# Kernel tuning notes

Hardware: AMD Instinct MI355X
Metric: run time of the kernel (lower is better)

Reference implementation:

```python
import jax, jax.numpy as jnp
import numpy as np

B, S, D = 4, 2048, 1024
H = 16
DK = D // H  # 64
F = 4096


def layer_norm(x, g, b, eps=1e-5):
    mu = jnp.mean(x, axis=-1, keepdims=True)
    var = jnp.mean(jnp.square(x - mu), axis=-1, keepdims=True)
    return (x - mu) * jax.lax.rsqrt(var + eps) * g + b


def setup_inputs() -> dict:
    key = jax.random.key(0)
    ks = jax.random.split(key, 12)
    s_in = 1.0 / np.sqrt(D)
    s_ff = 1.0 / np.sqrt(F)
    return {
        "x": jax.random.normal(ks[0], (B, S, D), jnp.float32),
        # per-head Q/K/V projections stacked: [H, D, DK]
        "Wq": jax.random.normal(ks[1], (H, D, DK), jnp.float32) * s_in,
        "bq": jnp.zeros((H, DK), jnp.float32),
        "Wk": jax.random.normal(ks[2], (H, D, DK), jnp.float32) * s_in,
        "bk": jnp.zeros((H, DK), jnp.float32),
        "Wv": jax.random.normal(ks[3], (H, D, DK), jnp.float32) * s_in,
        "bv": jnp.zeros((H, DK), jnp.float32),
        # output projection: [H*DK, D]
        "Wo": jax.random.normal(ks[4], (H * DK, D), jnp.float32) * s_in,
        "bo": jnp.zeros((D,), jnp.float32),
        "ln1_g": jnp.ones((D,), jnp.float32),
        "ln1_b": jnp.zeros((D,), jnp.float32),
        # FFN
        "W1": jax.random.normal(ks[5], (D, F), jnp.float32) * s_in,
        "b1": jnp.zeros((F,), jnp.float32),
        "W2": jax.random.normal(ks[6], (F, D), jnp.float32) * s_ff,
        "b2": jnp.zeros((D,), jnp.float32),
        "ln2_g": jnp.ones((D,), jnp.float32),
        "ln2_b": jnp.zeros((D,), jnp.float32),
    }


def reference(x, Wq, bq, Wk, bk, Wv, bv, Wo, bo, ln1_g, ln1_b,
              W1, b1, W2, b2, ln2_g, ln2_b):
    # --- multi-head attention (self-attention: q = k = v = x) ---
    q = jnp.einsum("bsd,hdk->bhsk", x, Wq) + bq[:, None, :]
    k = jnp.einsum("bsd,hdk->bhsk", x, Wk) + bk[:, None, :]
    v = jnp.einsum("bsd,hdk->bhsk", x, Wv) + bv[:, None, :]
    scale = 1.0 / jnp.sqrt(jnp.asarray(DK, x.dtype))
    scores = jnp.einsum("bhsk,bhtk->bhst", q, k) * scale  # [B,H,S,S]
    attn = jax.nn.softmax(scores, axis=-1)
    ctx = jnp.einsum("bhst,bhtk->bhsk", attn, v)           # [B,H,S,DK]
    # concat heads -> [B,S,H*DK], output projection
    ctx = jnp.transpose(ctx, (0, 2, 1, 3)).reshape(B, S, H * DK)
    attn_out = ctx @ Wo + bo
    # residual + post-LN (dropout is identity in eval mode)
    h = layer_norm(x + attn_out, ln1_g, ln1_b)
    # --- feed-forward (tanh activation) ---
    ff = jnp.tanh(h @ W1 + b1) @ W2 + b2
    return layer_norm(h + ff, ln2_g, ln2_b)
```

## Files before the change

### kernel.cpp

```cpp
#include <hip/hip_runtime.h>
#include <hip/hip_bf16.h>
#include <math.h>

typedef __attribute__((ext_vector_type(8))) short short8;
typedef __attribute__((ext_vector_type(4))) float f32x4;

#define NB 4
#define NS 2048
#define ND 1024
#define NH 16
#define NDK 64
#define NF 4096
#define NM (NB*NS)

#define QSCALE 0.18033688f
#define SMAX 32.0f

__device__ __forceinline__ unsigned short f2b(float f) {
  union { __hip_bfloat16 h; unsigned short u; } c;
  c.h = __float2bfloat16(f);
  return c.u;
}

__device__ __forceinline__ float b2f(unsigned short u) {
  union { float f; unsigned int i; } c;
  c.i = ((unsigned int)u) << 16;
  return c.f;
}

__device__ __forceinline__ void gload_lds16(const void* g, void* l) {
  __builtin_amdgcn_global_load_lds((const __attribute__((address_space(1))) void*)g,
                                   (__attribute__((address_space(3))) void*)l,
                                   16, 0, 0);
}

__device__ __forceinline__ float fast_tanh(float x) {
  float e = __builtin_amdgcn_exp2f(x * 2.885390082f);
  return 1.0f - 2.0f * __builtin_amdgcn_rcpf(e + 1.0f);
}


__global__ __launch_bounds__(256)
void cvt_f32_bf16(const float* __restrict__ in, unsigned short* __restrict__ out, int n4) {
  int i = blockIdx.x * 256 + threadIdx.x;
  if (i >= n4) return;
  float4 v = ((const float4*)in)[i];
  ushort4 o;
  o.x = f2b(v.x); o.y = f2b(v.y); o.z = f2b(v.z); o.w = f2b(v.w);
  ((ushort4*)out)[i] = o;
}

__global__ __launch_bounds__(256)
void transpose_generic(const float* __restrict__ src, unsigned short* __restrict__ dst,
                       int ldsrc, int lddst) {
  __shared__ float t[32][33];
  int k0 = blockIdx.x * 32, n0 = blockIdx.y * 32;
  int tx = threadIdx.x, ty = threadIdx.y;
  for (int r = ty; r < 32; r += 8)
    t[r][tx] = src[(size_t)(k0 + r) * ldsrc + n0 + tx];
  __syncthreads();
  for (int r = ty; r < 32; r += 8)
    dst[(size_t)(n0 + r) * lddst + k0 + tx] = f2b(t[tx][r]);
}

__global__ __launch_bounds__(256)
void transpose_qkv(const float* __restrict__ Wq, const float* __restrict__ Wk,
                   const float* __restrict__ Wv, unsigned short* __restrict__ dst) {
  int z = blockIdx.z, which = z / 16, h = z % 16;
  const float* src = (which == 0 ? Wq : which == 1 ? Wk : Wv) + (size_t)h * ND * NDK;
  float scale = (which == 0) ? QSCALE : 1.0f;
  unsigned short* d = dst + (size_t)(which * 1024 + h * 64) * ND;
  __shared__ float t[32][33];
  int k0 = blockIdx.x * 32, n0 = blockIdx.y * 32;
  int tx = threadIdx.x, ty = threadIdx.y;
  for (int r = ty; r < 32; r += 8)
    t[r][tx] = src[(size_t)(k0 + r) * NDK + n0 + tx];
  __syncthreads();
  for (int r = ty; r < 32; r += 8)
    d[(size_t)(n0 + r) * ND + k0 + tx] = f2b(t[tx][r] * scale);
}

__global__ __launch_bounds__(256)
void pack_bias(const float* __restrict__ bq, const float* __restrict__ bk,
               const float* __restrict__ bv, float* __restrict__ out) {
  int i = blockIdx.x * 256 + threadIdx.x;
  if (i >= 3072) return;
  float v = (i < 1024) ? bq[i] * QSCALE : (i < 2048 ? bk[i - 1024] : bv[i - 2048]);
  out[i] = v;
}

__global__ __launch_bounds__(256)
void transpose_v(const unsigned short* __restrict__ qkv, unsigned short* __restrict__ vt) {
  __shared__ unsigned short t[32][33];
  int bh = blockIdx.z; int b = bh >> 4, h = bh & 15;
  int s0 = blockIdx.x * 32;
  int d0 = blockIdx.y * 32;
  int tx = threadIdx.x, ty = threadIdx.y;
  for (int r = ty; r < 32; r += 8)
    t[r][tx] = qkv[(size_t)(b * NS + s0 + r) * 3072 + 2048 + h * 64 + d0 + tx];
  __syncthreads();
  for (int r = ty; r < 32; r += 8)
    vt[((size_t)bh * 64 + d0 + r) * NS + s0 + tx] = t[tx][r];
}


template<int EPI>
__global__ __launch_bounds__(256)
void gemm_bt(const unsigned short* __restrict__ A, const unsigned short* __restrict__ Bt,
             const float* __restrict__ bias, void* __restrict__ Cout,
             int M, int N, int K)
{
  __shared__ __align__(16) unsigned short As[128 * 64];
  __shared__ __align__(16) unsigned short Bs[128 * 64];

  const int id = blockIdx.x;
  const int xcd = id & 7;
  const int s = id >> 3;
  const int nbPerX = (N >> 7) >> 3;
  const int nb = xcd * nbPerX + (s % nbPerX);
  const int mb = s / nbPerX;
  const int n0 = nb * 128;
  const int m0 = mb * 128;

  const int tid = threadIdx.x;
  const int wave = tid >> 6, lane = tid & 63;
  const int l16 = lane & 15, lhi = lane >> 4;
  const int wr = wave >> 1, wc = wave & 1;

  const int rowL = lane >> 3;
  const int gg = (lane & 7) ^ rowL;
  const int ca = wave * 4;

  f32x4 acc[4][4] = {};

  for (int k0 = 0; k0 < K; k0 += 64) {
    __syncthreads();
#pragma unroll
    for (int c = ca; c < ca + 4; ++c) {
      gload_lds16(A + (size_t)(m0 + c * 8 + rowL) * K + (k0 + gg * 8), &As[c * 512]);
      gload_lds16(Bt + (size_t)(n0 + c * 8 + rowL) * K + (k0 + gg * 8), &Bs[c * 512]);
    }
    __syncthreads();

    short8 af[4][2], bf[4][2];
#pragma unroll
    for (int i = 0; i < 4; ++i) {
      const int row = wr * 64 + i * 16 + l16;
      const char* rb = (const char*)&As[row * 64];
#pragma unroll
      for (int ks = 0; ks < 2; ++ks)
        af[i][ks] = *(const short8*)(rb + (((ks * 4 + lhi) ^ (row & 7)) << 4));
    }
#pragma unroll
    for (int j = 0; j < 4; ++j) {
      const int row = wc * 64 + j * 16 + l16;
      const char* rb = (const char*)&Bs[row * 64];
#pragma unroll
      for (int ks = 0; ks < 2; ++ks)
        bf[j][ks] = *(const short8*)(rb + (((ks * 4 + lhi) ^ (row & 7)) << 4));
    }
#pragma unroll
    for (int i = 0; i < 4; ++i)
#pragma unroll
      for (int j = 0; j < 4; ++j)
#pragma unroll
        for (int ks = 0; ks < 2; ++ks)
          acc[i][j] = __builtin_amdgcn_mfma_f32_16x16x32_bf16(af[i][ks], bf[j][ks],
                                                              acc[i][j], 0, 0, 0);
  }

#pragma unroll
  for (int i = 0; i < 4; ++i) {
    const int row = m0 + wr * 64 + i * 16 + lhi * 4;
#pragma unroll
    for (int j = 0; j < 4; ++j) {
      const int col = n0 + wc * 64 + j * 16 + l16;
      const float bv = bias[col];
#pragma unroll
      for (int r = 0; r < 4; ++r) {
        float v = acc[i][j][r] + bv;
        size_t idx = (size_t)(row + r) * N + col;
        if (EPI == 0)      ((unsigned short*)Cout)[idx] = f2b(v);
        else if (EPI == 1) ((float*)Cout)[idx] = v;
        else               ((unsigned short*)Cout)[idx] = f2b(fast_tanh(v));
      }
    }
  }
}


__global__ __launch_bounds__(256)
void attn_fwd(const unsigned short* __restrict__ qkv, const unsigned short* __restrict__ vtg,
              unsigned short* __restrict__ ctx)
{
  const int id = blockIdx.x;
  const int swz = (id & 7) * 256 + (id >> 3);
  const int qt = swz & 31;
  const int bh = swz >> 5;
  const int b = bh >> 4, h = bh & 15;
  const int row0 = b * NS + qt * 64;
  const int tid = threadIdx.x;
  const int wave = tid >> 6, lane = tid & 63;
  const int l16 = lane & 15, lhi = lane >> 4;

  __shared__ __align__(16) unsigned short Ks[2][64 * 64];
  __shared__ __align__(16) unsigned short Vs[2][64 * 64];
  __shared__ __align__(16) unsigned short Ps[4][16 * 64];

  const unsigned short* kbase = qkv + ND + (size_t)h * 64;
  const unsigned short* vbase = vtg + (size_t)bh * 64 * NS;

  const int c0 = tid, c1 = 256 + tid;
  const int r0 = c0 >> 3, r1 = c1 >> 3;
  const int f0 = ((((c0 & 7) << 4) ^ ((r0 & 7) << 4)) >> 1);
  const int f1 = ((((c1 & 7) << 4) ^ ((r1 & 7) << 4)) >> 1);
  const int ldsb0 = wave * 512;
  const int ldsb1 = 2048 + wave * 512;

  short8 qf[2];
  {
    const unsigned short* qrow = qkv + (size_t)(row0 + wave * 16 + l16) * 3072 + h * 64;
    qf[0] = *(const short8*)(qrow + lhi * 8);
    qf[1] = *(const short8*)(qrow + 32 + lhi * 8);
  }

  f32x4 o[4] = {};
  float lr = 0.f;

  auto STAGE = [&](int buf, int kt) {
    const size_t kr = (size_t)(b * NS + kt * 64);
    const int kb64 = kt * 64;
    gload_lds16(kbase + (kr + r0) * 3072 + f0, &Ks[buf][ldsb0]);
    gload_lds16(kbase + (kr + r1) * 3072 + f1, &Ks[buf][ldsb1]);
    gload_lds16(vbase + (size_t)r0 * NS + kb64 + f0, &Vs[buf][ldsb0]);
    gload_lds16(vbase + (size_t)r1 * NS + kb64 + f1, &Vs[buf][ldsb1]);
  };

  auto COMPUTE = [&](int buf) {
    const char* kb = (const char*)&Ks[buf][0];
    const char* vb = (const char*)&Vs[buf][0];
    char* pb = (char*)&Ps[wave][0];

    f32x4 s[4] = {};
    __builtin_amdgcn_s_setprio(1);
#pragma unroll
    for (int c = 0; c < 2; ++c)
#pragma unroll
      for (int j = 0; j < 4; ++j) {
        const int row = j * 16 + l16;
        short8 kf = *(const short8*)(kb + row * 128 + ((c * 64 + lhi * 16) ^ ((row & 7) << 4)));
        s[j] = __builtin_amdgcn_mfma_f32_16x16x32_bf16(kf, qf[c], s[j], 0, 0, 0);
      }
    __builtin_amdgcn_s_setprio(0);

    float ls = 0.f;
#pragma unroll
    for (int j = 0; j < 4; ++j)
#pragma unroll
      for (int r = 0; r < 4; ++r) {
        float t = __builtin_amdgcn_exp2f(s[j][r] - SMAX);
        s[j][r] = t; ls += t;
      }
    lr += ls;

#pragma unroll
    for (int j = 0; j < 4; ++j)
#pragma unroll
      for (int rr = 0; rr < 2; ++rr) {
        unsigned int w = (unsigned int)f2b(s[j][2 * rr]) | ((unsigned int)f2b(s[j][2 * rr + 1]) << 16);
        *(unsigned int*)(pb + l16 * 128 + ((j * 32 + lhi * 8 + rr * 4) ^ ((l16 & 7) << 4))) = w;
      }

    __builtin_amdgcn_s_setprio(1);
#pragma unroll
    for (int c = 0; c < 2; ++c) {
      short8 pf = *(const short8*)(pb + l16 * 128 + ((c * 64 + lhi * 16) ^ ((l16 & 7) << 4)));
#pragma unroll
      for (int j = 0; j < 4; ++j) {
        const int row = j * 16 + l16;
        short8 vf = *(const short8*)(vb + row * 128 + ((c * 64 + lhi * 16) ^ ((row & 7) << 4)));
        o[j] = __builtin_amdgcn_mfma_f32_16x16x32_bf16(pf, vf, o[j], 0, 0, 0);
      }
    }
    __builtin_amdgcn_s_setprio(0);
  };

  STAGE(0, 0);
  __syncthreads();
  int cur = 0;
  for (int kt = 0; kt < NS / 64 - 1; ++kt) {
    STAGE(cur ^ 1, kt + 1);
    COMPUTE(cur);
    __syncthreads();
    cur ^= 1;
  }
  COMPUTE(cur);

  float t = lr;
  t += __shfl_xor(t, 16);
  t += __shfl_xor(t, 32);
  float rinv[4];
#pragma unroll
  for (int r = 0; r < 4; ++r) rinv[r] = 1.0f / __shfl(t, lhi * 4 + r);
#pragma unroll
  for (int j = 0; j < 4; ++j)
#pragma unroll
    for (int r = 0; r < 4; ++r) {
      const int row = row0 + wave * 16 + lhi * 4 + r;
      ctx[(size_t)row * ND + h * 64 + j * 16 + l16] = f2b(o[j][r] * rinv[r]);
    }
}


template<int MODE>
__global__ __launch_bounds__(256)
void ln_fused(const void* xa_, const void* xb_,
              const float* g, const float* beta, void* out_)
{
  const int row = blockIdx.x;
  const int tid = threadIdx.x;
  const int wave = tid >> 6, lane = tid & 63;
  __shared__ float r1[4], r2[4];

  float a0, a1, a2, a3;
  if (MODE == 0) {
    float4 a = ((const float4*)((const float*)xa_ + (size_t)row * ND))[tid];
    a0 = a.x; a1 = a.y; a2 = a.z; a3 = a.w;
  } else {
    ushort4 a = ((const ushort4*)((const unsigned short*)xa_ + (size_t)row * ND))[tid];
    a0 = b2f(a.x); a1 = b2f(a.y); a2 = b2f(a.z); a3 = b2f(a.w);
  }
  ushort4 bu = ((const ushort4*)((const unsigned short*)xb_ + (size_t)row * ND))[tid];
  float v0 = a0 + b2f(bu.x), v1 = a1 + b2f(bu.y), v2 = a2 + b2f(bu.z), v3 = a3 + b2f(bu.w);

  float sm = v0 + v1 + v2 + v3;
#pragma unroll
  for (int d = 1; d < 64; d <<= 1) sm += __shfl_xor(sm, d);
  if (lane == 0) r1[wave] = sm;
  __syncthreads();
  const float mu = (r1[0] + r1[1] + r1[2] + r1[3]) * (1.0f / ND);
  const float d0 = v0 - mu, d1 = v1 - mu, d2 = v2 - mu, d3 = v3 - mu;
  float vs = d0 * d0 + d1 * d1 + d2 * d2 + d3 * d3;
#pragma unroll
  for (int d = 1; d < 64; d <<= 1) vs += __shfl_xor(vs, d);
  if (lane == 0) r2[wave] = vs;
  __syncthreads();
  const float var = (r2[0] + r2[1] + r2[2] + r2[3]) * (1.0f / ND);
  const float inv = rsqrtf(var + 1e-5f);
  float4 gg = ((const float4*)g)[tid];
  float4 bb = ((const float4*)beta)[tid];
  float o0 = d0 * inv * gg.x + bb.x;
  float o1 = d1 * inv * gg.y + bb.y;
  float o2 = d2 * inv * gg.z + bb.z;
  float o3 = d3 * inv * gg.w + bb.w;
  if (MODE == 0) {
    ushort4 w; w.x = f2b(o0); w.y = f2b(o1); w.z = f2b(o2); w.w = f2b(o3);
    ((ushort4*)((unsigned short*)out_ + (size_t)row * ND))[tid] = w;
  } else {
    float4 ov; ov.x = o0; ov.y = o1; ov.z = o2; ov.w = o3;
    ((float4*)((float*)out_ + (size_t)row * ND))[tid] = ov;
  }
}


extern "C" void kernel_launch(void* const* d_in, const int* in_sizes, int n_in,
                              void* d_out, int out_size, void* d_ws, size_t ws_size,
                              hipStream_t stream)
{
  (void)in_sizes; (void)n_in; (void)out_size; (void)ws_size;
  const float* x   = (const float*)d_in[0];
  const float* Wq  = (const float*)d_in[1];
  const float* bq  = (const float*)d_in[2];
  const float* Wk  = (const float*)d_in[3];
  const float* bk  = (const float*)d_in[4];
  const float* Wv  = (const float*)d_in[5];
  const float* bv  = (const float*)d_in[6];
  const float* Wo  = (const float*)d_in[7];
  const float* bo  = (const float*)d_in[8];
  const float* g1  = (const float*)d_in[9];
  const float* be1 = (const float*)d_in[10];
  const float* W1  = (const float*)d_in[11];
  const float* b1  = (const float*)d_in[12];
  const float* W2  = (const float*)d_in[13];
  const float* b2  = (const float*)d_in[14];
  const float* g2  = (const float*)d_in[15];
  const float* be2 = (const float*)d_in[16];

  char* ws = (char*)d_ws;
  const size_t MB = 1ull << 20;
  unsigned short* x_bf  = (unsigned short*)(ws);
  unsigned short* vtg   = (unsigned short*)(ws);
  unsigned short* qkv   = (unsigned short*)(ws + 16 * MB);
  unsigned short* aout  = (unsigned short*)(ws + 16 * MB);
  unsigned short* ff1   = (unsigned short*)(ws);
  unsigned short* ctx   = (unsigned short*)(ws + 64 * MB);
  unsigned short* h_bf  = (unsigned short*)(ws + 64 * MB);
  unsigned short* Wqkvt = (unsigned short*)(ws + 80 * MB);
  unsigned short* Wot   = (unsigned short*)(ws + 86 * MB);
  unsigned short* W1t   = (unsigned short*)(ws + 88 * MB);
  unsigned short* W2t   = (unsigned short*)(ws + 96 * MB);
  float*          bqkv  = (float*)(ws + 104 * MB);
  unsigned short* ffout = (unsigned short*)(ws + 105 * MB);

  cvt_f32_bf16<<<NM * ND / 4 / 256, 256, 0, stream>>>(x, x_bf, NM * ND / 4);
  transpose_qkv<<<dim3(32, 2, 48), dim3(32, 8), 0, stream>>>(Wq, Wk, Wv, Wqkvt);
  transpose_generic<<<dim3(32, 32), dim3(32, 8), 0, stream>>>(Wo, Wot, 1024, 1024);
  transpose_generic<<<dim3(32, 128), dim3(32, 8), 0, stream>>>(W1, W1t, 4096, 1024);
  transpose_generic<<<dim3(128, 32), dim3(32, 8), 0, stream>>>(W2, W2t, 1024, 4096);
  pack_bias<<<12, 256, 0, stream>>>(bq, bk, bv, bqkv);

  gemm_bt<0><<<(NM / 128) * (3072 / 128), 256, 0, stream>>>(x_bf, Wqkvt, bqkv, qkv, NM, 3072, 1024);
  transpose_v<<<dim3(64, 2, 64), dim3(32, 8), 0, stream>>>(qkv, vtg);
  attn_fwd<<<2048, 256, 0, stream>>>(qkv, vtg, ctx);
  gemm_bt<0><<<(NM / 128) * (1024 / 128), 256, 0, stream>>>(ctx, Wot, bo, aout, NM, 1024, 1024);
  ln_fused<0><<<NM, 256, 0, stream>>>(x, aout, g1, be1, h_bf);
  gemm_bt<2><<<(NM / 128) * (4096 / 128), 256, 0, stream>>>(h_bf, W1t, b1, ff1, NM, 4096, 1024);
  gemm_bt<0><<<(NM / 128) * (1024 / 128), 256, 0, stream>>>(ff1, W2t, b2, ffout, NM, 1024, 4096);
  ln_fused<1><<<NM, 256, 0, stream>>>(h_bf, ffout, g2, be2, (float*)d_out);
}
```

Measured before the change: 481.9 us.

## Double-buffer GEMM LDS tiles and enlarge attention blocks to 128 queries

The GEMM now keeps two LDS buffers, so the next K tile loads while MFMAs run on the current one, with one barrier per iteration instead of two and raised priority around the MFMA block. The attention kernel goes from 256 to 512 threads and 64 to 128 query rows per block, and each thread now issues a single K/V staging load per tile. This lets more waves share each staged K/V tile and halves K/V reloads. The cost is double the GEMM LDS footprint, which may lower occupancy, and different scheduling behaviour for the larger attention blocks.

```diff
diff --git a/kernel.cpp b/kernel.cpp
--- a/kernel.cpp
+++ b/kernel.cpp
@@ -110,8 +110,8 @@
              const float* __restrict__ bias, void* __restrict__ Cout,
              int M, int N, int K)
 {
-  __shared__ __align__(16) unsigned short As[128 * 64];
-  __shared__ __align__(16) unsigned short Bs[128 * 64];
+  __shared__ __align__(16) unsigned short As[2][128 * 64];
+  __shared__ __align__(16) unsigned short Bs[2][128 * 64];
 
   const int id = blockIdx.x;
   const int xcd = id & 7;
@@ -133,20 +133,23 @@
 
   f32x4 acc[4][4] = {};
 
-  for (int k0 = 0; k0 < K; k0 += 64) {
-    __syncthreads();
+  auto STAGE = [&](int buf, int kt) {
+    const int k0 = kt * 64;
 #pragma unroll
     for (int c = ca; c < ca + 4; ++c) {
-      gload_lds16(A + (size_t)(m0 + c * 8 + rowL) * K + (k0 + gg * 8), &As[c * 512]);
-      gload_lds16(Bt + (size_t)(n0 + c * 8 + rowL) * K + (k0 + gg * 8), &Bs[c * 512]);
-    }
-    __syncthreads();
-
+      gload_lds16(A + (size_t)(m0 + c * 8 + rowL) * K + (k0 + gg * 8), &As[buf][c * 512]);
+      gload_lds16(Bt + (size_t)(n0 + c * 8 + rowL) * K + (k0 + gg * 8), &Bs[buf][c * 512]);
+    }
+  };
+
+  auto COMPUTE = [&](int buf) {
+    const char* as = (const char*)&As[buf][0];
+    const char* bs = (const char*)&Bs[buf][0];
     short8 af[4][2], bf[4][2];
 #pragma unroll
     for (int i = 0; i < 4; ++i) {
       const int row = wr * 64 + i * 16 + l16;
-      const char* rb = (const char*)&As[row * 64];
+      const char* rb = as + row * 128;
 #pragma unroll
       for (int ks = 0; ks < 2; ++ks)
         af[i][ks] = *(const short8*)(rb + (((ks * 4 + lhi) ^ (row & 7)) << 4));
@@ -154,11 +157,12 @@
 #pragma unroll
     for (int j = 0; j < 4; ++j) {
       const int row = wc * 64 + j * 16 + l16;
-      const char* rb = (const char*)&Bs[row * 64];
+      const char* rb = bs + row * 128;
 #pragma unroll
       for (int ks = 0; ks < 2; ++ks)
         bf[j][ks] = *(const short8*)(rb + (((ks * 4 + lhi) ^ (row & 7)) << 4));
     }
+    __builtin_amdgcn_s_setprio(1);
 #pragma unroll
     for (int i = 0; i < 4; ++i)
 #pragma unroll
@@ -167,7 +171,20 @@
         for (int ks = 0; ks < 2; ++ks)
           acc[i][j] = __builtin_amdgcn_mfma_f32_16x16x32_bf16(af[i][ks], bf[j][ks],
                                                               acc[i][j], 0, 0, 0);
-  }
+    __builtin_amdgcn_s_setprio(0);
+  };
+
+  const int NT = K >> 6;
+  STAGE(0, 0);
+  __syncthreads();
+  int cur = 0;
+  for (int kt = 0; kt < NT - 1; ++kt) {
+    STAGE(cur ^ 1, kt + 1);
+    COMPUTE(cur);
+    __syncthreads();
+    cur ^= 1;
+  }
+  COMPUTE(cur);
 
 #pragma unroll
   for (int i = 0; i < 4; ++i) {
@@ -189,33 +206,30 @@
 }
 
 
-__global__ __launch_bounds__(256)
+__global__ __launch_bounds__(512)
 void attn_fwd(const unsigned short* __restrict__ qkv, const unsigned short* __restrict__ vtg,
               unsigned short* __restrict__ ctx)
 {
   const int id = blockIdx.x;
-  const int swz = (id & 7) * 256 + (id >> 3);
-  const int qt = swz & 31;
-  const int bh = swz >> 5;
+  const int swz = (id & 7) * 128 + (id >> 3);
+  const int qt = swz & 15;
+  const int bh = swz >> 4;
   const int b = bh >> 4, h = bh & 15;
-  const int row0 = b * NS + qt * 64;
+  const int row0 = b * NS + qt * 128;
   const int tid = threadIdx.x;
   const int wave = tid >> 6, lane = tid & 63;
   const int l16 = lane & 15, lhi = lane >> 4;
 
   __shared__ __align__(16) unsigned short Ks[2][64 * 64];
   __shared__ __align__(16) unsigned short Vs[2][64 * 64];
-  __shared__ __align__(16) unsigned short Ps[4][16 * 64];
+  __shared__ __align__(16) unsigned short Ps[8][16 * 64];
 
   const unsigned short* kbase = qkv + ND + (size_t)h * 64;
   const unsigned short* vbase = vtg + (size_t)bh * 64 * NS;
 
-  const int c0 = tid, c1 = 256 + tid;
-  const int r0 = c0 >> 3, r1 = c1 >> 3;
-  const int f0 = ((((c0 & 7) << 4) ^ ((r0 & 7) << 4)) >> 1);
-  const int f1 = ((((c1 & 7) << 4) ^ ((r1 & 7) << 4)) >> 1);
+  const int r0 = tid >> 3;
+  const int f0 = ((tid & 7) ^ (r0 & 7)) * 8;
   const int ldsb0 = wave * 512;
-  const int ldsb1 = 2048 + wave * 512;
 
   short8 qf[2];
   {
@@ -231,9 +245,7 @@
     const size_t kr = (size_t)(b * NS + kt * 64);
     const int kb64 = kt * 64;
     gload_lds16(kbase + (kr + r0) * 3072 + f0, &Ks[buf][ldsb0]);
-    gload_lds16(kbase + (kr + r1) * 3072 + f1, &Ks[buf][ldsb1]);
     gload_lds16(vbase + (size_t)r0 * NS + kb64 + f0, &Vs[buf][ldsb0]);
-    gload_lds16(vbase + (size_t)r1 * NS + kb64 + f1, &Vs[buf][ldsb1]);
   };
 
   auto COMPUTE = [&](int buf) {
@@ -411,7 +423,7 @@
 
   gemm_bt<0><<<(NM / 128) * (3072 / 128), 256, 0, stream>>>(x_bf, Wqkvt, bqkv, qkv, NM, 3072, 1024);
   transpose_v<<<dim3(64, 2, 64), dim3(32, 8), 0, stream>>>(qkv, vtg);
-  attn_fwd<<<2048, 256, 0, stream>>>(qkv, vtg, ctx);
+  attn_fwd<<<1024, 512, 0, stream>>>(qkv, vtg, ctx);
   gemm_bt<0><<<(NM / 128) * (1024 / 128), 256, 0, stream>>>(ctx, Wot, bo, aout, NM, 1024, 1024);
   ln_fused<0><<<NM, 256, 0, stream>>>(x, aout, g1, be1, h_bf);
   gemm_bt<2><<<(NM / 128) * (4096 / 128), 256, 0, stream>>>(h_bf, W1t, b1, ff1, NM, 4096, 1024);
```

Result: faster. 458.9 us (-4.8%).
